# Optimization experiments

Hardware: AMD Instinct MI355X
Metric: run time of the kernel (lower is better)

## Reference

```python
import jax, jax.numpy as jnp
import numpy as np

B, C, H, W = 64, 64, 64, 64
KD = 64  # kernel_dim == res == dim (required by the torch reshapes)


def _ln(t, g, b, eps=1e-5):
    mu = jnp.mean(t, axis=-1, keepdims=True)
    var = jnp.var(t, axis=-1, keepdims=True)
    return (t - mu) * jax.lax.rsqrt(var + eps) * g + b


def _cos_map(n, kd):
    i = jnp.arange(n, dtype=jnp.float32)[:, None]
    j = jnp.arange(kd, dtype=jnp.float32)[None, :]
    return jnp.cos(i * j * jnp.pi / n) / kd


def setup_inputs() -> dict:
    key = jax.random.key(0)
    ks = jax.random.split(key, 6)
    s = 0.02
    return {
        "x": jax.random.normal(ks[0], (B, C, H, W), jnp.float32),
        "freq_embed": jax.random.normal(ks[1], (H, W, C), jnp.float32),
        "g_k": jnp.ones((C,), jnp.float32), "b_k": jnp.zeros((C,), jnp.float32),
        "Wk": jax.random.normal(ks[2], (C, KD), jnp.float32) * s, "bk": jnp.zeros((KD,), jnp.float32),
        "g_z": jnp.ones((C,), jnp.float32), "b_z": jnp.zeros((C,), jnp.float32),
        "Wz": jax.random.normal(ks[3], (C, C), jnp.float32) * s, "bz": jnp.zeros((C,), jnp.float32),
        "g_o": jnp.ones((KD,), jnp.float32), "b_o": jnp.zeros((KD,), jnp.float32),
        "Wo": jax.random.normal(ks[4], (KD, C), jnp.float32) * s, "bo": jnp.zeros((C,), jnp.float32),
    }


def reference(x, freq_embed, g_k, b_k, Wk, bk, g_z, b_z, Wz, bz, g_o, b_o, Wo, bo):
    # x: (B,C,H,W) -> (B,H,W,C), matching the torch permute branch
    x = jnp.transpose(x, (0, 2, 3, 1))
    Bc, Hc, Wc, Cc = x.shape
    kd = Wk.shape[1]
    xin = x + freq_embed[None]                    # freq_embed broadcast over batch
    k = _ln(xin, g_k, b_k) @ Wk + bk              # (B,H,W,kd)
    z = _ln(freq_embed, g_z, b_z) @ Wz + bz       # to_k(freq_embed): (H,W,C)
    cosn = _cos_map(Hc, kd)                       # (H,kd)
    cosm = _cos_map(Wc, kd)                       # (W,kd)
    i = jnp.arange(Hc, dtype=jnp.float32)[:, None]
    j = jnp.arange(Wc, dtype=jnp.float32)[None, :]
    decay = (jnp.exp(-(i + j) / max(Hc, Wc)) / kd).astype(x.dtype)  # (H,W)
    wexp = decay[:, :, None] ** z                 # (H,W,C), decay > 0
    # separable forward DCT (two kernel-1 conv1d == two contractions)
    t = jnp.einsum('nh,bhwc->bnwc', cosn, k)
    t = jnp.einsum('mw,bnwc->bnmc', cosm, t)
    t = t * wexp[None]                            # exponential-decay spectral gate
    # separable inverse DCT
    t = jnp.einsum('nh,bnmc->bhmc', cosn, t)
    t = jnp.einsum('mw,bhmc->bhwc', cosm, t)
    out = _ln(t, g_o, b_o) * jax.nn.silu(z)[None]
    out = out @ Wo + bo
    return jnp.transpose(out, (0, 3, 1, 2))       # back to BCHW
```

## Files before the change

### kernel.cpp

```cpp
#include <hip/hip_runtime.h>


#define PL_ST 4160
#define TC_ST 4160

typedef __attribute__((ext_vector_type(8))) short short8;
typedef __attribute__((ext_vector_type(4))) float f32x4;
typedef __attribute__((ext_vector_type(4))) unsigned short us4;

__device__ __forceinline__ unsigned short bfhi(float f) {
    return (unsigned short)(__builtin_bit_cast(unsigned int, f) >> 16);
}
__device__ __forceinline__ float hif(float f) {
    return __builtin_bit_cast(float, __builtin_bit_cast(unsigned int, f) & 0xFFFF0000u);
}
__device__ __forceinline__ int swa(int row, int col) {
    return (row << 7) + (((col >> 3) ^ (row & 7)) << 4) + ((col & 7) << 1);
}
__device__ __forceinline__ short8 fragrd(const short* buf, int row, int kc) {
    int a = (row << 7) + ((kc ^ (row & 7)) << 4);
    return *(const short8*)((const char*)buf + a);
}
__device__ __forceinline__ f32x4 mm3(short8 ah, short8 al, short8 bh, short8 bl, f32x4 acc) {
    acc = __builtin_amdgcn_mfma_f32_16x16x32_bf16(ah, bh, acc, 0, 0, 0);
    acc = __builtin_amdgcn_mfma_f32_16x16x32_bf16(ah, bl, acc, 0, 0, 0);
    acc = __builtin_amdgcn_mfma_f32_16x16x32_bf16(al, bh, acc, 0, 0, 0);
    return acc;
}

__device__ __forceinline__ void mm_block(const short* Ah, const short* Al,
                                         const short* Bh, const short* Bl,
                                         int m0, int n0, int l15, int q,
                                         f32x4 (&acc)[2][2]) {
    const f32x4 zero = {0.f, 0.f, 0.f, 0.f};
    acc[0][0] = zero; acc[0][1] = zero; acc[1][0] = zero; acc[1][1] = zero;
    #pragma unroll
    for (int kb = 0; kb < 2; ++kb) {
        int kc = (kb << 2) + q;
        short8 a0h = fragrd(Ah, m0 + l15, kc);
        short8 a0l = fragrd(Al, m0 + l15, kc);
        short8 a1h = fragrd(Ah, m0 + 16 + l15, kc);
        short8 a1l = fragrd(Al, m0 + 16 + l15, kc);
        short8 b0h = fragrd(Bh, n0 + l15, kc);
        short8 b0l = fragrd(Bl, n0 + l15, kc);
        short8 b1h = fragrd(Bh, n0 + 16 + l15, kc);
        short8 b1l = fragrd(Bl, n0 + 16 + l15, kc);
        acc[0][0] = mm3(a0h, a0l, b0h, b0l, acc[0][0]);
        acc[0][1] = mm3(a0h, a0l, b1h, b1l, acc[0][1]);
        acc[1][0] = mm3(a1h, a1l, b0h, b0l, acc[1][0]);
        acc[1][1] = mm3(a1h, a1l, b1h, b1l, acc[1][1]);
    }
}

__device__ __forceinline__ void mm_block_regB(const short* Ah, const short* Al,
                                              const short8 (&bf)[2][2][2],
                                              int m0, int l15, int q,
                                              f32x4 (&acc)[2][2]) {
    const f32x4 zero = {0.f, 0.f, 0.f, 0.f};
    acc[0][0] = zero; acc[0][1] = zero; acc[1][0] = zero; acc[1][1] = zero;
    #pragma unroll
    for (int kb = 0; kb < 2; ++kb) {
        int kc = (kb << 2) + q;
        short8 a0h = fragrd(Ah, m0 + l15, kc);
        short8 a0l = fragrd(Al, m0 + l15, kc);
        short8 a1h = fragrd(Ah, m0 + 16 + l15, kc);
        short8 a1l = fragrd(Al, m0 + 16 + l15, kc);
        #pragma unroll
        for (int u = 0; u < 2; ++u) {
            acc[0][u] = mm3(a0h, a0l, bf[u][kb][0], bf[u][kb][1], acc[0][u]);
            acc[1][u] = mm3(a1h, a1l, bf[u][kb][0], bf[u][kb][1], acc[1][u]);
        }
    }
}

__global__ __launch_bounds__(256) void k_pre1(
    const float* __restrict__ g_k, const float* __restrict__ b_k,
    const float* __restrict__ Wk, const float* __restrict__ bk,
    const float* __restrict__ g_z, const float* __restrict__ b_z,
    const float* __restrict__ Wz, const float* __restrict__ bz,
    const float* __restrict__ Wo,
    unsigned short* __restrict__ WkTh, unsigned short* __restrict__ WkTl,
    float* __restrict__ su_k, float* __restrict__ v_k,
    unsigned short* __restrict__ WzTh, unsigned short* __restrict__ WzTl,
    float* __restrict__ su_z, float* __restrict__ v_z,
    unsigned short* __restrict__ WoTh, unsigned short* __restrict__ WoTl,
    unsigned short* __restrict__ cos_hi, unsigned short* __restrict__ cos_lo) {
    int t = threadIdx.x;
    if (blockIdx.x < 16) {
        int n = blockIdx.x * 4 + (t >> 6);
        int c = t & 63;
        float wk = Wk[c * 64 + n];
        float a = g_k[c] * wk;
        WkTh[n * 64 + c] = bfhi(a);
        WkTl[n * 64 + c] = bfhi(a - hif(a));
        float sa = a, sv = b_k[c] * wk;
        #pragma unroll
        for (int off = 32; off > 0; off >>= 1) {
            sa += __shfl_xor(sa, off, 64);
            sv += __shfl_xor(sv, off, 64);
        }
        if (c == 0) { su_k[n] = sa; v_k[n] = sv + bk[n]; }
        float wz = Wz[c * 64 + n];
        float az = g_z[c] * wz;
        WzTh[n * 64 + c] = bfhi(az);
        WzTl[n * 64 + c] = bfhi(az - hif(az));
        float saz = az, svz = b_z[c] * wz;
        #pragma unroll
        for (int off = 32; off > 0; off >>= 1) {
            saz += __shfl_xor(saz, off, 64);
            svz += __shfl_xor(svz, off, 64);
        }
        if (c == 0) { su_z[n] = saz; v_z[n] = svz + bz[n]; }
        float wo = Wo[c * 64 + n];
        WoTh[n * 64 + c] = bfhi(wo);
        WoTl[n * 64 + c] = bfhi(wo - hif(wo));
    } else {
        int idx = (blockIdx.x - 16) * 256 + t;
        int i = idx >> 6, j = idx & 63;
        float ang = (float)(i * j) * 3.14159265358979323846f * (1.0f / 64.0f);
        float v = cosf(ang) * (1.0f / 64.0f);
        cos_hi[idx] = bfhi(v);
        cos_lo[idx] = bfhi(v - hif(v));
    }
}

__global__ __launch_bounds__(256) void k_pre2(
    const float* __restrict__ freq,
    const unsigned short* __restrict__ WzTh_g, const unsigned short* __restrict__ WzTl_g,
    const float* __restrict__ su_z, const float* __restrict__ v_z,
    float* __restrict__ siluzT, float* __restrict__ wexpT,
    float* __restrict__ freqT) {
    __shared__ __align__(16) short Ah[4096], Al[4096], Bh[4096], Bl[4096];
    __shared__ float muS[64], rsS[64];
    __shared__ float tile[64][65];
    int t = threadIdx.x;
    if (blockIdx.x < 64) {
        int h = blockIdx.x;
        #pragma unroll
        for (int p = 0; p < 2; ++p) {
            int e = t + p * 256;
            int row = e >> 3, ch = e & 7;
            int a = (row << 7) + (((ch ^ (row & 7)) << 4));
            *(uint4*)((char*)Bh + a) = *(const uint4*)&WzTh_g[row * 64 + ch * 8];
            *(uint4*)((char*)Bl + a) = *(const uint4*)&WzTl_g[row * 64 + ch * 8];
        }
        int w = t >> 2, c0 = (t & 3) << 4;
        float4 fr[4];
        float s1 = 0.f, s2 = 0.f;
        #pragma unroll
        for (int i = 0; i < 4; ++i) {
            fr[i] = *(const float4*)&freq[(h * 64 + w) * 64 + c0 + 4 * i];
            s1 += fr[i].x + fr[i].y + fr[i].z + fr[i].w;
            s2 += fr[i].x * fr[i].x + fr[i].y * fr[i].y + fr[i].z * fr[i].z + fr[i].w * fr[i].w;
        }
        s1 += __shfl_xor(s1, 1, 64); s1 += __shfl_xor(s1, 2, 64);
        s2 += __shfl_xor(s2, 1, 64); s2 += __shfl_xor(s2, 2, 64);
        float mu = s1 * (1.0f / 64.0f);
        float var = s2 * (1.0f / 64.0f) - mu * mu;
        float rs = rsqrtf(var + 1e-5f);
        if ((t & 3) == 0) { muS[w] = mu; rsS[w] = rs; }
        const float* fp = (const float*)fr;
        #pragma unroll
        for (int i = 0; i < 4; ++i) {
            us4 hv, lv;
            #pragma unroll
            for (int r = 0; r < 4; ++r) {
                float f = fp[i * 4 + r];
                hv[r] = bfhi(f);
                lv[r] = bfhi(f - hif(f));
            }
            int a = swa(w, c0 + 4 * i);
            *(us4*)((char*)Ah + a) = hv;
            *(us4*)((char*)Al + a) = lv;
        }
        __syncthreads();
        int lane = t & 63, wv = t >> 6;
        int q = lane >> 4, l15 = lane & 15;
        int m0 = (wv & 1) << 5, n0 = (wv >> 1) << 5;
        f32x4 acc[2][2];
        mm_block(Ah, Al, Bh, Bl, m0, n0, l15, q, acc);
        #pragma unroll
        for (int u = 0; u < 2; ++u) {
            int c = n0 + (u << 4) + l15;
            float suc = su_z[c], vc = v_z[c];
            #pragma unroll
            for (int ti = 0; ti < 2; ++ti) {
                int wb = m0 + (ti << 4) + (q << 2);
                float4 mu4 = *(const float4*)&muS[wb];
                float4 rs4 = *(const float4*)&rsS[wb];
                float4 sil, wx;
                #pragma unroll
                for (int r = 0; r < 4; ++r) {
                    float z = ((const float*)&rs4)[r] * (acc[ti][u][r] - ((const float*)&mu4)[r] * suc) + vc;
                    float lnd = -(float)(h + wb + r) * 0.015625f - 4.1588830833596718565f;
                    ((float*)&sil)[r] = z / (1.0f + expf(-z));
                    ((float*)&wx)[r] = expf(z * lnd);
                }
                size_t base = (size_t)c * TC_ST + h * 64 + wb;
                *(float4*)&siluzT[base] = sil;
                *(float4*)&wexpT[base] = wx;
            }
        }
    } else {
        int h = blockIdx.x - 64;
        int w = t >> 2, c0 = (t & 3) << 4;
        #pragma unroll
        for (int i = 0; i < 4; ++i)
            *(float4*)&tile[w][c0 + 4 * i] = *(const float4*)&freq[(h * 64 + w) * 64 + c0 + 4 * i];
        __syncthreads();
        int w0 = (t & 15) << 2;
        #pragma unroll
        for (int p = 0; p < 4; ++p) {
            int c = (t >> 4) + 16 * p;
            float4 fv = make_float4(tile[w0][c], tile[w0 + 1][c], tile[w0 + 2][c], tile[w0 + 3][c]);
            *(float4*)&freqT[(size_t)c * TC_ST + h * 64 + w0] = fv;
        }
    }
}

__global__ __launch_bounds__(256, 3) void k_k(
    const float* __restrict__ x, const float* __restrict__ freqT,
    const unsigned short* __restrict__ WkTh_g, const unsigned short* __restrict__ WkTl_g,
    const float* __restrict__ su_k, const float* __restrict__ v_k,
    float* __restrict__ planes) {
    __shared__ __align__(16) short Ah[2][4096], Al[2][4096];
    __shared__ __align__(16) float red1[4][64], red2[4][64];
    __shared__ float muS[64], rsS[64];
    int b = blockIdx.x >> 4, h0 = (blockIdx.x & 15) << 2;
    int t = threadIdx.x;
    int lane = t & 63, wv = t >> 6;
    int q = lane >> 4, l15 = lane & 15;
    int m0 = (wv & 1) << 5, n0 = (wv >> 1) << 5;
    short8 bf[2][2][2];
    #pragma unroll
    for (int u = 0; u < 2; ++u)
        #pragma unroll
        for (int kb = 0; kb < 2; ++kb) {
            int off = (n0 + (u << 4) + l15) * 64 + ((kb << 2) + q) * 8;
            bf[u][kb][0] = *(const short8*)&WkTh_g[off];
            bf[u][kb][1] = *(const short8*)&WkTl_g[off];
        }
    int g = t >> 4, w0 = (t & 15) << 2, c0 = g << 2;
    const float* xb = x + (size_t)b * 262144;
    float4 xr[2][4], fr[2][4];
    #pragma unroll
    for (int pi = 0; pi < 2; ++pi) {
        int h = h0 + pi;
        #pragma unroll
        for (int i = 0; i < 4; ++i) {
            xr[pi][i] = *(const float4*)&xb[(c0 + i) * 4096 + h * 64 + w0];
            fr[pi][i] = *(const float4*)&freqT[(size_t)(c0 + i) * TC_ST + h * 64 + w0];
        }
    }
    #pragma unroll
    for (int it = 0; it < 4; ++it) {
        int s = it & 1;
        int h = h0 + it;
        float4 vv[4];
        float4 s1 = {0, 0, 0, 0}, s2 = {0, 0, 0, 0};
        #pragma unroll
        for (int i = 0; i < 4; ++i) {
            float4 a = xr[s][i], f = fr[s][i];
            a.x += f.x; a.y += f.y; a.z += f.z; a.w += f.w;
            vv[i] = a;
            s1.x += a.x; s1.y += a.y; s1.z += a.z; s1.w += a.w;
            s2.x += a.x * a.x; s2.y += a.y * a.y; s2.z += a.z * a.z; s2.w += a.w * a.w;
        }
        const float* vp = (const float*)vv;
        #pragma unroll
        for (int j = 0; j < 4; ++j) {
            us4 hv, lv;
            #pragma unroll
            for (int r = 0; r < 4; ++r) {
                float f = vp[r * 4 + j];
                hv[r] = bfhi(f);
                lv[r] = bfhi(f - hif(f));
            }
            int a = swa(w0 + j, c0);
            *(us4*)((char*)Ah[s] + a) = hv;
            *(us4*)((char*)Al[s] + a) = lv;
        }
        #pragma unroll
        for (int r = 0; r < 4; ++r) {
            float a1 = ((const float*)&s1)[r];
            float a2 = ((const float*)&s2)[r];
            a1 += __shfl_xor(a1, 16, 64); a1 += __shfl_xor(a1, 32, 64);
            a2 += __shfl_xor(a2, 16, 64); a2 += __shfl_xor(a2, 32, 64);
            ((float*)&s1)[r] = a1;
            ((float*)&s2)[r] = a2;
        }
        if (lane < 16) {
            *(float4*)&red1[wv][lane << 2] = s1;
            *(float4*)&red2[wv][lane << 2] = s2;
        }
        __syncthreads();
        if (t < 64) {
            float a1 = red1[0][t] + red1[1][t] + red1[2][t] + red1[3][t];
            float a2 = red2[0][t] + red2[1][t] + red2[2][t] + red2[3][t];
            float mu = a1 * (1.0f / 64.0f);
            float var = a2 * (1.0f / 64.0f) - mu * mu;
            muS[t] = mu; rsS[t] = rsqrtf(var + 1e-5f);
        }
        __syncthreads();
        if (it < 2) {
            int hn = h0 + it + 2;
            #pragma unroll
            for (int i = 0; i < 4; ++i) {
                xr[s][i] = *(const float4*)&xb[(c0 + i) * 4096 + hn * 64 + w0];
                fr[s][i] = *(const float4*)&freqT[(size_t)(c0 + i) * TC_ST + hn * 64 + w0];
            }
        }
        f32x4 acc[2][2];
        mm_block_regB(Ah[s], Al[s], bf, m0, l15, q, acc);
        #pragma unroll
        for (int u = 0; u < 2; ++u) {
            int n = n0 + (u << 4) + l15;
            float sun = su_k[n], vn = v_k[n];
            #pragma unroll
            for (int ti = 0; ti < 2; ++ti) {
                int wb = m0 + (ti << 4) + (q << 2);
                float4 mu4 = *(const float4*)&muS[wb];
                float4 rs4 = *(const float4*)&rsS[wb];
                float4 o;
                o.x = rs4.x * (acc[ti][u][0] - mu4.x * sun) + vn;
                o.y = rs4.y * (acc[ti][u][1] - mu4.y * sun) + vn;
                o.z = rs4.z * (acc[ti][u][2] - mu4.z * sun) + vn;
                o.w = rs4.w * (acc[ti][u][3] - mu4.w * sun) + vn;
                *(float4*)&planes[(size_t)(b * 64 + n) * PL_ST + h * 64 + wb] = o;
            }
        }
    }
}

__global__ __launch_bounds__(256, 4) void k_spec(
    float* __restrict__ planes,
    const unsigned short* __restrict__ cos_hi, const unsigned short* __restrict__ cos_lo,
    const float* __restrict__ wexpT) {
    __shared__ __align__(16) short Ch[4096], Cl[4096];
    __shared__ __align__(16) short Dh[4096], Dl[4096];
    int c = blockIdx.x & 63;
    float* po = planes + (size_t)blockIdx.x * PL_ST;
    const float* wx = wexpT + (size_t)c * TC_ST;
    int t = threadIdx.x;
    int lane = t & 63, wv = t >> 6;
    int q = lane >> 4, l15 = lane & 15;
    int m0 = (wv & 1) << 5, n0 = (wv >> 1) << 5;

    float wxr[2][2][4];
    #pragma unroll
    for (int ti = 0; ti < 2; ++ti)
        #pragma unroll
        for (int u = 0; u < 2; ++u)
            #pragma unroll
            for (int r = 0; r < 4; ++r)
                wxr[ti][u][r] = wx[(m0 + (ti << 4) + (q << 2) + r) * 64
                                   + n0 + (u << 4) + l15];

    {
        int r = t >> 2, cb = (t & 3) << 4;
        #pragma unroll
        for (int p = 0; p < 2; ++p) {
            int chunk = (cb >> 3) + p;
            int a = (r << 7) + (((chunk ^ (r & 7)) << 4));
            *(uint4*)((char*)Ch + a) = *(const uint4*)&cos_hi[r * 64 + cb + p * 8];
            *(uint4*)((char*)Cl + a) = *(const uint4*)&cos_lo[r * 64 + cb + p * 8];
        }
    }
    {
        int w = t & 63, h0 = (t >> 6) << 4;
        float v[16];
        #pragma unroll
        for (int j = 0; j < 16; ++j) v[j] = po[(h0 + j) * 64 + w];
        #pragma unroll
        for (int gg = 0; gg < 4; ++gg) {
            int col = h0 + (gg << 2);
            int a = swa(w, col);
            us4 hv, lv;
            #pragma unroll
            for (int r = 0; r < 4; ++r) {
                float f = v[(gg << 2) + r];
                hv[r] = bfhi(f);
                lv[r] = bfhi(f - hif(f));
            }
            *(us4*)((char*)Dh + a) = hv;
            *(us4*)((char*)Dl + a) = lv;
        }
    }
    __syncthreads();

    short8 af[2][2][2];
    f32x4 acc[2][2];
    const f32x4 zacc = {0.f, 0.f, 0.f, 0.f};

#define LOAD_D(base)                                                          \
    _Pragma("unroll")                                                         \
    for (int tt = 0; tt < 2; ++tt)                                            \
        _Pragma("unroll")                                                     \
        for (int kb = 0; kb < 2; ++kb) {                                      \
            af[tt][kb][0] = fragrd(Dh, (base) + (tt << 4) + l15, (kb << 2) + q); \
            af[tt][kb][1] = fragrd(Dl, (base) + (tt << 4) + l15, (kb << 2) + q); \
        }

#define QMM_AC()                                                              \
    acc[0][0] = zacc; acc[0][1] = zacc; acc[1][0] = zacc; acc[1][1] = zacc;   \
    __builtin_amdgcn_s_setprio(1);                                            \
    _Pragma("unroll")                                                         \
    for (int kb = 0; kb < 2; ++kb) {                                          \
        int kc = (kb << 2) + q;                                               \
        short8 b0h = fragrd(Ch, n0 + l15, kc);                                \
        short8 b0l = fragrd(Cl, n0 + l15, kc);                                \
        short8 b1h = fragrd(Ch, n0 + 16 + l15, kc);                           \
        short8 b1l = fragrd(Cl, n0 + 16 + l15, kc);                           \
        acc[0][0] = mm3(af[0][kb][0], af[0][kb][1], b0h, b0l, acc[0][0]);     \
        acc[0][1] = mm3(af[0][kb][0], af[0][kb][1], b1h, b1l, acc[0][1]);     \
        acc[1][0] = mm3(af[1][kb][0], af[1][kb][1], b0h, b0l, acc[1][0]);     \
        acc[1][1] = mm3(af[1][kb][0], af[1][kb][1], b1h, b1l, acc[1][1]);     \
    }                                                                         \
    __builtin_amdgcn_s_setprio(0);

#define QMM_CA()                                                              \
    acc[0][0] = zacc; acc[0][1] = zacc; acc[1][0] = zacc; acc[1][1] = zacc;   \
    __builtin_amdgcn_s_setprio(1);                                            \
    _Pragma("unroll")                                                         \
    for (int kb = 0; kb < 2; ++kb) {                                          \
        int kc = (kb << 2) + q;                                               \
        short8 a0h = fragrd(Ch, m0 + l15, kc);                                \
        short8 a0l = fragrd(Cl, m0 + l15, kc);                                \
        short8 a1h = fragrd(Ch, m0 + 16 + l15, kc);                           \
        short8 a1l = fragrd(Cl, m0 + 16 + l15, kc);                           \
        acc[0][0] = mm3(a0h, a0l, af[0][kb][0], af[0][kb][1], acc[0][0]);     \
        acc[0][1] = mm3(a0h, a0l, af[1][kb][0], af[1][kb][1], acc[0][1]);     \
        acc[1][0] = mm3(a1h, a1l, af[0][kb][0], af[0][kb][1], acc[1][0]);     \
        acc[1][1] = mm3(a1h, a1l, af[1][kb][0], af[1][kb][1], acc[1][1]);     \
    }                                                                         \
    __builtin_amdgcn_s_setprio(0);

#define WB_T()                                                                \
    _Pragma("unroll")                                                         \
    for (int ti = 0; ti < 2; ++ti)                                            \
        _Pragma("unroll")                                                     \
        for (int u = 0; u < 2; ++u) {                                         \
            int row = n0 + (u << 4) + l15;                                    \
            int col = m0 + (ti << 4) + (q << 2);                              \
            int a = swa(row, col);                                            \
            us4 hv, lv;                                                       \
            _Pragma("unroll")                                                 \
            for (int r = 0; r < 4; ++r) {                                     \
                float f = acc[ti][u][r];                                      \
                hv[r] = bfhi(f);                                              \
                lv[r] = bfhi(f - hif(f));                                     \
            }                                                                 \
            *(us4*)((char*)Dh + a) = hv;                                      \
            *(us4*)((char*)Dl + a) = lv;                                      \
        }

    LOAD_D(m0)
    __syncthreads();
    QMM_AC()
    WB_T()
    __syncthreads();

    LOAD_D(m0)
    __syncthreads();
    QMM_AC()
    #pragma unroll
    for (int ti = 0; ti < 2; ++ti)
        #pragma unroll
        for (int u = 0; u < 2; ++u)
            #pragma unroll
            for (int r = 0; r < 4; ++r)
                acc[ti][u][r] *= wxr[ti][u][r];
    WB_T()
    __syncthreads();

    LOAD_D(n0)
    __syncthreads();
    QMM_CA()
    #pragma unroll
    for (int ti = 0; ti < 2; ++ti)
        #pragma unroll
        for (int u = 0; u < 2; ++u)
            #pragma unroll
            for (int r = 0; r < 4; ++r) {
                int row = m0 + (ti << 4) + (q << 2) + r;
                int col = n0 + (u << 4) + l15;
                int a = swa(row, col);
                float f = acc[ti][u][r];
                *(unsigned short*)((char*)Dh + a) = bfhi(f);
                *(unsigned short*)((char*)Dl + a) = bfhi(f - hif(f));
            }
    __syncthreads();

    LOAD_D(m0)
    __syncthreads();
    QMM_AC()
    #pragma unroll
    for (int ti = 0; ti < 2; ++ti)
        #pragma unroll
        for (int u = 0; u < 2; ++u)
            #pragma unroll
            for (int r = 0; r < 4; ++r) {
                int h = m0 + (ti << 4) + (q << 2) + r;
                int w = n0 + (u << 4) + l15;
                po[h * 64 + w] = acc[ti][u][r];
            }
#undef LOAD_D
#undef QMM_AC
#undef QMM_CA
#undef WB_T
}

__global__ __launch_bounds__(256, 3) void k_out(
    const float* __restrict__ planes, const float* __restrict__ siluzT,
    const float* __restrict__ g_o, const float* __restrict__ b_o,
    const unsigned short* __restrict__ WoTh_g, const unsigned short* __restrict__ WoTl_g,
    const float* __restrict__ bo, float* __restrict__ out) {
    __shared__ __align__(16) short Ah[2][4096], Al[2][4096];
    __shared__ __align__(16) float red1[4][64], red2[4][64];
    __shared__ float muS[64], rsS[64];
    int b = blockIdx.x >> 4, h0 = (blockIdx.x & 15) << 2;
    int t = threadIdx.x;
    int lane = t & 63, wv = t >> 6;
    int q = lane >> 4, l15 = lane & 15;
    int m0 = (wv & 1) << 5, n0 = (wv >> 1) << 5;
    short8 bf[2][2][2];
    #pragma unroll
    for (int u = 0; u < 2; ++u)
        #pragma unroll
        for (int kb = 0; kb < 2; ++kb) {
            int off = (n0 + (u << 4) + l15) * 64 + ((kb << 2) + q) * 8;
            bf[u][kb][0] = *(const short8*)&WoTh_g[off];
            bf[u][kb][1] = *(const short8*)&WoTl_g[off];
        }
    int g = t >> 4, w0 = (t & 15) << 2, c0 = g << 2;
    float4 pr[2][4], sz[2][4];
    #pragma unroll
    for (int pi = 0; pi < 2; ++pi) {
        int h = h0 + pi;
        #pragma unroll
        for (int i = 0; i < 4; ++i) {
            pr[pi][i] = *(const float4*)&planes[(size_t)(b * 64 + c0 + i) * PL_ST + h * 64 + w0];
            sz[pi][i] = *(const float4*)&siluzT[(size_t)(c0 + i) * TC_ST + h * 64 + w0];
        }
    }
    #pragma unroll
    for (int it = 0; it < 4; ++it) {
        int s = it & 1;
        int h = h0 + it;
        float4 s1 = {0, 0, 0, 0}, s2 = {0, 0, 0, 0};
        #pragma unroll
        for (int i = 0; i < 4; ++i) {
            float4 tv = pr[s][i];
            s1.x += tv.x; s1.y += tv.y; s1.z += tv.z; s1.w += tv.w;
            s2.x += tv.x * tv.x; s2.y += tv.y * tv.y;
            s2.z += tv.z * tv.z; s2.w += tv.w * tv.w;
        }
        #pragma unroll
        for (int r = 0; r < 4; ++r) {
            float a1 = ((const float*)&s1)[r];
            float a2 = ((const float*)&s2)[r];
            a1 += __shfl_xor(a1, 16, 64); a1 += __shfl_xor(a1, 32, 64);
            a2 += __shfl_xor(a2, 16, 64); a2 += __shfl_xor(a2, 32, 64);
            ((float*)&s1)[r] = a1;
            ((float*)&s2)[r] = a2;
        }
        if (lane < 16) {
            *(float4*)&red1[wv][lane << 2] = s1;
            *(float4*)&red2[wv][lane << 2] = s2;
        }
        __syncthreads();
        if (t < 64) {
            float a1 = red1[0][t] + red1[1][t] + red1[2][t] + red1[3][t];
            float a2 = red2[0][t] + red2[1][t] + red2[2][t] + red2[3][t];
            float mu = a1 * (1.0f / 64.0f);
            float var = a2 * (1.0f / 64.0f) - mu * mu;
            muS[t] = mu; rsS[t] = rsqrtf(var + 1e-5f);
        }
        __syncthreads();
        {
            float4 mu4 = *(const float4*)&muS[w0];
            float4 rs4 = *(const float4*)&rsS[w0];
            float4 vr[4];
            #pragma unroll
            for (int i = 0; i < 4; ++i) {
                int cc = c0 + i;
                float go = g_o[cc], boc = b_o[cc];
                float4 tv = pr[s][i], sv = sz[s][i];
                vr[i].x = ((tv.x - mu4.x) * rs4.x * go + boc) * sv.x;
                vr[i].y = ((tv.y - mu4.y) * rs4.y * go + boc) * sv.y;
                vr[i].z = ((tv.z - mu4.z) * rs4.z * go + boc) * sv.z;
                vr[i].w = ((tv.w - mu4.w) * rs4.w * go + boc) * sv.w;
            }
            const float* vp = (const float*)vr;
            #pragma unroll
            for (int j = 0; j < 4; ++j) {
                us4 hv, lv;
                #pragma unroll
                for (int r = 0; r < 4; ++r) {
                    float f = vp[r * 4 + j];
                    hv[r] = bfhi(f);
                    lv[r] = bfhi(f - hif(f));
                }
                int a = swa(w0 + j, c0);
                *(us4*)((char*)Ah[s] + a) = hv;
                *(us4*)((char*)Al[s] + a) = lv;
            }
        }
        if (it < 2) {
            int hn = h0 + it + 2;
            #pragma unroll
            for (int i = 0; i < 4; ++i) {
                pr[s][i] = *(const float4*)&planes[(size_t)(b * 64 + c0 + i) * PL_ST + hn * 64 + w0];
                sz[s][i] = *(const float4*)&siluzT[(size_t)(c0 + i) * TC_ST + hn * 64 + w0];
            }
        }
        __syncthreads();
        f32x4 acc[2][2];
        mm_block_regB(Ah[s], Al[s], bf, m0, l15, q, acc);
        #pragma unroll
        for (int u = 0; u < 2; ++u) {
            int o_ = n0 + (u << 4) + l15;
            float bov = bo[o_];
            #pragma unroll
            for (int ti = 0; ti < 2; ++ti) {
                int wb = m0 + (ti << 4) + (q << 2);
                float4 o;
                o.x = acc[ti][u][0] + bov;
                o.y = acc[ti][u][1] + bov;
                o.z = acc[ti][u][2] + bov;
                o.w = acc[ti][u][3] + bov;
                *(float4*)&out[((size_t)(b * 64 + o_) * 64 + h) * 64 + wb] = o;
            }
        }
    }
}

extern "C" void kernel_launch(void* const* d_in, const int* in_sizes, int n_in,
                              void* d_out, int out_size, void* d_ws, size_t ws_size,
                              hipStream_t stream) {
    const float* x    = (const float*)d_in[0];
    const float* freq = (const float*)d_in[1];
    const float* g_k  = (const float*)d_in[2];
    const float* b_k  = (const float*)d_in[3];
    const float* Wk   = (const float*)d_in[4];
    const float* bk   = (const float*)d_in[5];
    const float* g_z  = (const float*)d_in[6];
    const float* b_z  = (const float*)d_in[7];
    const float* Wz   = (const float*)d_in[8];
    const float* bz   = (const float*)d_in[9];
    const float* g_o  = (const float*)d_in[10];
    const float* b_o  = (const float*)d_in[11];
    const float* Wo   = (const float*)d_in[12];
    const float* bo   = (const float*)d_in[13];
    float* out = (float*)d_out;

    float* ws = (float*)d_ws;
    float* planes = ws;
    float* siluzT = planes + (size_t)4096 * PL_ST;
    float* wexpT  = siluzT + (size_t)64 * TC_ST;
    float* freqT  = wexpT + (size_t)64 * TC_ST;
    float* su_k   = freqT + (size_t)64 * TC_ST;
    float* v_k    = su_k + 64;
    float* su_z   = v_k + 64;
    float* v_z    = su_z + 64;
    unsigned short* cos_hi = (unsigned short*)(v_z + 64);
    unsigned short* cos_lo = cos_hi + 4096;
    unsigned short* WkTh = cos_lo + 4096;
    unsigned short* WkTl = WkTh + 4096;
    unsigned short* WzTh = WkTl + 4096;
    unsigned short* WzTl = WzTh + 4096;
    unsigned short* WoTh = WzTl + 4096;
    unsigned short* WoTl = WoTh + 4096;

    k_pre1<<<32, 256, 0, stream>>>(g_k, b_k, Wk, bk, g_z, b_z, Wz, bz, Wo,
                                   WkTh, WkTl, su_k, v_k, WzTh, WzTl, su_z, v_z,
                                   WoTh, WoTl, cos_hi, cos_lo);
    k_pre2<<<128, 256, 0, stream>>>(freq, WzTh, WzTl, su_z, v_z, siluzT, wexpT, freqT);
    k_k<<<1024, 256, 0, stream>>>(x, freqT, WkTh, WkTl, su_k, v_k, planes);
    k_spec<<<4096, 256, 0, stream>>>(planes, cos_hi, cos_lo, wexpT);
    k_out<<<1024, 256, 0, stream>>>(planes, siluzT, g_o, b_o, WoTh, WoTl, bo, out);
}
```

Before: 228.8 us.

## Store planes h-major and round-to-nearest in bf16 hi/lo splits

Changes the intermediate planes buffer from per-(b,c) slabs to per-(b,h) slabs, so the k-producing and output kernels write and read contiguous channel rows for a fixed h. The DCT kernel now reads and writes with a PL_ST row stride instead. It also replaces truncating bf16 hi/lo splitting with round-to-nearest-even, which improves the accuracy of the 3-MFMA emulation but adds a few integer ops per conversion. Access coalescing moves from the producer/consumer kernels to the strided DCT kernel, so the net effect depends on which side was the bottleneck.

```diff
diff --git a/kernel.cpp b/kernel.cpp
--- a/kernel.cpp
+++ b/kernel.cpp
@@ -8,11 +8,16 @@
 typedef __attribute__((ext_vector_type(4))) float f32x4;
 typedef __attribute__((ext_vector_type(4))) unsigned short us4;
 
-__device__ __forceinline__ unsigned short bfhi(float f) {
-    return (unsigned short)(__builtin_bit_cast(unsigned int, f) >> 16);
-}
-__device__ __forceinline__ float hif(float f) {
-    return __builtin_bit_cast(float, __builtin_bit_cast(unsigned int, f) & 0xFFFF0000u);
+__device__ __forceinline__ unsigned short bfrnd(float f) {
+    unsigned int u = __builtin_bit_cast(unsigned int, f);
+    u += 0x7FFFu + ((u >> 16) & 1u);
+    return (unsigned short)(u >> 16);
+}
+__device__ __forceinline__ void bfsplit(float f, unsigned short& hi, unsigned short& lo) {
+    unsigned short h = bfrnd(f);
+    float fh = __builtin_bit_cast(float, (unsigned int)h << 16);
+    hi = h;
+    lo = bfrnd(f - fh);
 }
 __device__ __forceinline__ int swa(int row, int col) {
     return (row << 7) + (((col >> 3) ^ (row & 7)) << 4) + ((col & 7) << 1);
@@ -89,10 +94,12 @@
     if (blockIdx.x < 16) {
         int n = blockIdx.x * 4 + (t >> 6);
         int c = t & 63;
+        unsigned short h_, l_;
         float wk = Wk[c * 64 + n];
         float a = g_k[c] * wk;
-        WkTh[n * 64 + c] = bfhi(a);
-        WkTl[n * 64 + c] = bfhi(a - hif(a));
+        bfsplit(a, h_, l_);
+        WkTh[n * 64 + c] = h_;
+        WkTl[n * 64 + c] = l_;
         float sa = a, sv = b_k[c] * wk;
         #pragma unroll
         for (int off = 32; off > 0; off >>= 1) {
@@ -102,8 +109,9 @@
         if (c == 0) { su_k[n] = sa; v_k[n] = sv + bk[n]; }
         float wz = Wz[c * 64 + n];
         float az = g_z[c] * wz;
-        WzTh[n * 64 + c] = bfhi(az);
-        WzTl[n * 64 + c] = bfhi(az - hif(az));
+        bfsplit(az, h_, l_);
+        WzTh[n * 64 + c] = h_;
+        WzTl[n * 64 + c] = l_;
         float saz = az, svz = b_z[c] * wz;
         #pragma unroll
         for (int off = 32; off > 0; off >>= 1) {
@@ -112,15 +120,18 @@
         }
         if (c == 0) { su_z[n] = saz; v_z[n] = svz + bz[n]; }
         float wo = Wo[c * 64 + n];
-        WoTh[n * 64 + c] = bfhi(wo);
-        WoTl[n * 64 + c] = bfhi(wo - hif(wo));
+        bfsplit(wo, h_, l_);
+        WoTh[n * 64 + c] = h_;
+        WoTl[n * 64 + c] = l_;
     } else {
         int idx = (blockIdx.x - 16) * 256 + t;
         int i = idx >> 6, j = idx & 63;
         float ang = (float)(i * j) * 3.14159265358979323846f * (1.0f / 64.0f);
         float v = cosf(ang) * (1.0f / 64.0f);
-        cos_hi[idx] = bfhi(v);
-        cos_lo[idx] = bfhi(v - hif(v));
+        unsigned short h_, l_;
+        bfsplit(v, h_, l_);
+        cos_hi[idx] = h_;
+        cos_lo[idx] = l_;
     }
 }
 
@@ -165,9 +176,10 @@
             us4 hv, lv;
             #pragma unroll
             for (int r = 0; r < 4; ++r) {
-                float f = fp[i * 4 + r];
-                hv[r] = bfhi(f);
-                lv[r] = bfhi(f - hif(f));
+                unsigned short h_, l_;
+                bfsplit(fp[i * 4 + r], h_, l_);
+                hv[r] = h_;
+                lv[r] = l_;
             }
             int a = swa(w, c0 + 4 * i);
             *(us4*)((char*)Ah + a) = hv;
@@ -272,9 +284,10 @@
             us4 hv, lv;
             #pragma unroll
             for (int r = 0; r < 4; ++r) {
-                float f = vp[r * 4 + j];
-                hv[r] = bfhi(f);
-                lv[r] = bfhi(f - hif(f));
+                unsigned short h_, l_;
+                bfsplit(vp[r * 4 + j], h_, l_);
+                hv[r] = h_;
+                lv[r] = l_;
             }
             int a = swa(w0 + j, c0);
             *(us4*)((char*)Ah[s] + a) = hv;
@@ -312,6 +325,7 @@
         }
         f32x4 acc[2][2];
         mm_block_regB(Ah[s], Al[s], bf, m0, l15, q, acc);
+        float* slab = planes + (size_t)(b * 64 + h) * PL_ST;
         #pragma unroll
         for (int u = 0; u < 2; ++u) {
             int n = n0 + (u << 4) + l15;
@@ -326,7 +340,7 @@
                 o.y = rs4.y * (acc[ti][u][1] - mu4.y * sun) + vn;
                 o.z = rs4.z * (acc[ti][u][2] - mu4.z * sun) + vn;
                 o.w = rs4.w * (acc[ti][u][3] - mu4.w * sun) + vn;
-                *(float4*)&planes[(size_t)(b * 64 + n) * PL_ST + h * 64 + wb] = o;
+                *(float4*)&slab[n * 64 + wb] = o;
             }
         }
     }
@@ -338,8 +352,9 @@
     const float* __restrict__ wexpT) {
     __shared__ __align__(16) short Ch[4096], Cl[4096];
     __shared__ __align__(16) short Dh[4096], Dl[4096];
-    int c = blockIdx.x & 63;
-    float* po = planes + (size_t)blockIdx.x * PL_ST;
+    int bid = blockIdx.x;
+    int b = bid >> 6, c = bid & 63;
+    float* pb = planes + (size_t)b * 64 * PL_ST + c * 64;
     const float* wx = wexpT + (size_t)c * TC_ST;
     int t = threadIdx.x;
     int lane = t & 63, wv = t >> 6;
@@ -370,7 +385,7 @@
         int w = t & 63, h0 = (t >> 6) << 4;
         float v[16];
         #pragma unroll
-        for (int j = 0; j < 16; ++j) v[j] = po[(h0 + j) * 64 + w];
+        for (int j = 0; j < 16; ++j) v[j] = pb[(size_t)(h0 + j) * PL_ST + w];
         #pragma unroll
         for (int gg = 0; gg < 4; ++gg) {
             int col = h0 + (gg << 2);
@@ -378,9 +393,10 @@
             us4 hv, lv;
             #pragma unroll
             for (int r = 0; r < 4; ++r) {
-                float f = v[(gg << 2) + r];
-                hv[r] = bfhi(f);
-                lv[r] = bfhi(f - hif(f));
+                unsigned short h_, l_;
+                bfsplit(v[(gg << 2) + r], h_, l_);
+                hv[r] = h_;
+                lv[r] = l_;
             }
             *(us4*)((char*)Dh + a) = hv;
             *(us4*)((char*)Dl + a) = lv;
@@ -446,9 +462,10 @@
             us4 hv, lv;                                                       \
             _Pragma("unroll")                                                 \
             for (int r = 0; r < 4; ++r) {                                     \
-                float f = acc[ti][u][r];                                      \
-                hv[r] = bfhi(f);                                              \
-                lv[r] = bfhi(f - hif(f));                                     \
+                unsigned short h_, l_;                                        \
+                bfsplit(acc[ti][u][r], h_, l_);                               \
+                hv[r] = h_;                                                   \
+                lv[r] = l_;                                                   \
             }                                                                 \
             *(us4*)((char*)Dh + a) = hv;                                      \
             *(us4*)((char*)Dl + a) = lv;                                      \
@@ -485,9 +502,10 @@
                 int row = m0 + (ti << 4) + (q << 2) + r;
                 int col = n0 + (u << 4) + l15;
                 int a = swa(row, col);
-                float f = acc[ti][u][r];
-                *(unsigned short*)((char*)Dh + a) = bfhi(f);
-                *(unsigned short*)((char*)Dl + a) = bfhi(f - hif(f));
+                unsigned short h_, l_;
+                bfsplit(acc[ti][u][r], h_, l_);
+                *(unsigned short*)((char*)Dh + a) = h_;
+                *(unsigned short*)((char*)Dl + a) = l_;
             }
     __syncthreads();
 
@@ -502,7 +520,7 @@
             for (int r = 0; r < 4; ++r) {
                 int h = m0 + (ti << 4) + (q << 2) + r;
                 int w = n0 + (u << 4) + l15;
-                po[h * 64 + w] = acc[ti][u][r];
+                pb[(size_t)h * PL_ST + w] = acc[ti][u][r];
             }
 #undef LOAD_D
 #undef QMM_AC
@@ -537,9 +555,10 @@
     #pragma unroll
     for (int pi = 0; pi < 2; ++pi) {
         int h = h0 + pi;
+        const float* slab = planes + (size_t)(b * 64 + h) * PL_ST;
         #pragma unroll
         for (int i = 0; i < 4; ++i) {
-            pr[pi][i] = *(const float4*)&planes[(size_t)(b * 64 + c0 + i) * PL_ST + h * 64 + w0];
+            pr[pi][i] = *(const float4*)&slab[(c0 + i) * 64 + w0];
             sz[pi][i] = *(const float4*)&siluzT[(size_t)(c0 + i) * TC_ST + h * 64 + w0];
         }
     }
@@ -597,9 +616,10 @@
                 us4 hv, lv;
                 #pragma unroll
                 for (int r = 0; r < 4; ++r) {
-                    float f = vp[r * 4 + j];
-                    hv[r] = bfhi(f);
-                    lv[r] = bfhi(f - hif(f));
+                    unsigned short h_, l_;
+                    bfsplit(vp[r * 4 + j], h_, l_);
+                    hv[r] = h_;
+                    lv[r] = l_;
                 }
                 int a = swa(w0 + j, c0);
                 *(us4*)((char*)Ah[s] + a) = hv;
@@ -608,9 +628,10 @@
         }
         if (it < 2) {
             int hn = h0 + it + 2;
+            const float* slab = planes + (size_t)(b * 64 + hn) * PL_ST;
             #pragma unroll
             for (int i = 0; i < 4; ++i) {
-                pr[s][i] = *(const float4*)&planes[(size_t)(b * 64 + c0 + i) * PL_ST + hn * 64 + w0];
+                pr[s][i] = *(const float4*)&slab[(c0 + i) * 64 + w0];
                 sz[s][i] = *(const float4*)&siluzT[(size_t)(c0 + i) * TC_ST + hn * 64 + w0];
             }
         }
```

Result: faster. 222.8 us (-2.6%).
